# Kernel optimization log

Hardware: AMD Instinct MI355X
Metric: run time of the kernel (lower is better)

Reference implementation:

```python
import jax, jax.numpy as jnp
import numpy as np

INPUT_DIM = 512
SLOT_DIM = 256
MEM_SLOTS = 64

def setup_inputs() -> dict:
    key = jax.random.key(0)
    ks = jax.random.split(key, 6)
    B, S = 16, 4096
    sequence = jax.random.normal(ks[0], (B, S, INPUT_DIM), dtype=jnp.float32)
    # encoder Linear(input_dim -> slot_dim)
    enc_w = jax.random.normal(ks[1], (SLOT_DIM, INPUT_DIM), dtype=jnp.float32) / np.sqrt(INPUT_DIM)
    enc_b = jnp.zeros((SLOT_DIM,), dtype=jnp.float32)
    # memory bank
    mem = jax.random.normal(ks[2], (MEM_SLOTS, SLOT_DIM), dtype=jnp.float32) * 0.1
    # decoder Linear(slot_dim -> input_dim)
    dec_w = jax.random.normal(ks[3], (INPUT_DIM, SLOT_DIM), dtype=jnp.float32) / np.sqrt(SLOT_DIM)
    dec_b = jnp.zeros((INPUT_DIM,), dtype=jnp.float32)
    return {"sequence": sequence, "enc_w": enc_w, "enc_b": enc_b,
            "mem": mem, "dec_w": dec_w, "dec_b": dec_b}

def reference(sequence, enc_w, enc_b, mem, dec_w, dec_b):
    # encode: [B,S,D] @ [D,Dk] -> tanh
    encoded = jnp.tanh(jnp.einsum('bsd,kd->bsk', sequence, enc_w) + enc_b)
    scale = jnp.sqrt(jnp.asarray(encoded.shape[-1], encoded.dtype))
    # attention over memory slots: [B,S,M]
    attention = jax.nn.softmax(jnp.einsum('bsk,mk->bsm', encoded, mem) / scale, axis=-1)
    # weighted read: [B,S,Dk]
    memory = jnp.einsum('bsm,mk->bsk', attention, mem)
    # decode: [B,S,D]
    reconstruction = jnp.einsum('bsk,dk->bsd', memory, dec_w) + dec_b
    return reconstruction, attention, memory
```

## Files before the change

kernel.cpp:

```cpp
#include <hip/hip_runtime.h>

#define IN_DIM  512
#define SL_DIM  256
#define M_SLOTS 64
#define TILE_R  64

typedef __attribute__((ext_vector_type(8))) short  short8;
typedef __attribute__((ext_vector_type(4))) float  f32x4;

__device__ __forceinline__ short f2bf(float f) {
  union { float f; unsigned u; } v; v.f = f;
  unsigned r = (v.u + 0x7FFFu + ((v.u >> 16) & 1u)) >> 16;
  return (short)r;
}

__device__ __forceinline__ float fast_tanh(float x) {
  x = fminf(15.f, fmaxf(-15.f, x));
  float e = __expf(2.f * x);
  return (e - 1.f) / (e + 1.f);
}

__global__ void convert_weights(const float* __restrict__ enc_w,
                                const float* __restrict__ dec_w,
                                const float* __restrict__ mem,
                                short* __restrict__ encb, short* __restrict__ decb,
                                short* __restrict__ memb, short* __restrict__ memTb) {
  int i = blockIdx.x * 256 + threadIdx.x;
  encb[i] = f2bf(enc_w[i]);
  decb[i] = f2bf(dec_w[i]);
  if (i < M_SLOTS * SL_DIM) {
    short v = f2bf(mem[i]);
    memb[i] = v;
    memTb[(i & 255) * M_SLOTS + (i >> 8)] = v;
  }
}

__global__ __launch_bounds__(256, 3) void fused_kernel(
    const float* __restrict__ seq, const float* __restrict__ enc_b,
    const float* __restrict__ dec_b, const short* __restrict__ encw,
    const short* __restrict__ decw, const short* __restrict__ memb,
    const short* __restrict__ memTb, float* __restrict__ out) {
  const int tid  = threadIdx.x;
  const int wave = tid >> 6;
  const int lane = tid & 63;
  const int l16  = lane & 15;
  const int quad = lane >> 4;
  const int r0   = blockIdx.x * TILE_R;

  __shared__ __align__(16) short As[TILE_R][40];
  __shared__ __align__(16) short Ebuf[TILE_R][SL_DIM + 8];
  __shared__ __align__(16) short Pbuf[TILE_R][M_SLOTS + 8];

  float* __restrict__ outR = out;
  float* __restrict__ outA = out + 33554432;
  float* __restrict__ outM = out + 37748736;

  f32x4 acc[4][4];
#pragma unroll
  for (int rb = 0; rb < 4; ++rb)
#pragma unroll
    for (int cb = 0; cb < 4; ++cb) acc[rb][cb] = (f32x4){0.f, 0.f, 0.f, 0.f};

  const int srow = tid >> 2;
  const int skc  = (tid & 3) * 8;
  const float* sp = seq + (size_t)(r0 + srow) * IN_DIM + skc;

  for (int kt = 0; kt < 16; ++kt) {
    const int k0 = kt * 32;
    float4 v0 = *(const float4*)(sp + k0);
    float4 v1 = *(const float4*)(sp + k0 + 4);
    short8 s;
    s[0] = f2bf(v0.x); s[1] = f2bf(v0.y); s[2] = f2bf(v0.z); s[3] = f2bf(v0.w);
    s[4] = f2bf(v1.x); s[5] = f2bf(v1.y); s[6] = f2bf(v1.z); s[7] = f2bf(v1.w);
    __syncthreads();
    *(short8*)&As[srow][skc] = s;
    __syncthreads();
    short8 a[4], b[4];
#pragma unroll
    for (int rb = 0; rb < 4; ++rb)
      a[rb] = *(const short8*)&As[16 * rb + l16][quad * 8];
#pragma unroll
    for (int cb = 0; cb < 4; ++cb) {
      int n = 64 * wave + 16 * cb + l16;
      b[cb] = *(const short8*)(encw + n * IN_DIM + k0 + quad * 8);
    }
#pragma unroll
    for (int rb = 0; rb < 4; ++rb)
#pragma unroll
      for (int cb = 0; cb < 4; ++cb)
        acc[rb][cb] = __builtin_amdgcn_mfma_f32_16x16x32_bf16(a[rb], b[cb], acc[rb][cb], 0, 0, 0);
  }

#pragma unroll
  for (int cb = 0; cb < 4; ++cb) {
    int col = 64 * wave + 16 * cb + l16;
    float bias = enc_b[col];
#pragma unroll
    for (int rb = 0; rb < 4; ++rb)
#pragma unroll
      for (int r = 0; r < 4; ++r) {
        int row = 16 * rb + quad * 4 + r;
        Ebuf[row][col] = f2bf(fast_tanh(acc[rb][cb][r] + bias));
      }
  }
  __syncthreads();

  f32x4 acc2[4];
#pragma unroll
  for (int nb = 0; nb < 4; ++nb) acc2[nb] = (f32x4){0.f, 0.f, 0.f, 0.f};
  const int g2row = 16 * wave + l16;
#pragma unroll
  for (int kt = 0; kt < 8; ++kt) {
    int k0 = kt * 32;
    short8 a = *(const short8*)&Ebuf[g2row][k0 + quad * 8];
#pragma unroll
    for (int nb = 0; nb < 4; ++nb) {
      short8 b = *(const short8*)(memb + (16 * nb + l16) * SL_DIM + k0 + quad * 8);
      acc2[nb] = __builtin_amdgcn_mfma_f32_16x16x32_bf16(a, b, acc2[nb], 0, 0, 0);
    }
  }
#pragma unroll
  for (int r = 0; r < 4; ++r) {
    int lrow = 16 * wave + quad * 4 + r;
    float s0 = acc2[0][r] * 0.0625f, s1 = acc2[1][r] * 0.0625f;
    float s2 = acc2[2][r] * 0.0625f, s3 = acc2[3][r] * 0.0625f;
    float mx = fmaxf(fmaxf(s0, s1), fmaxf(s2, s3));
    for (int off = 1; off < 16; off <<= 1) mx = fmaxf(mx, __shfl_xor(mx, off));
    float e0 = __expf(s0 - mx), e1 = __expf(s1 - mx);
    float e2 = __expf(s2 - mx), e3 = __expf(s3 - mx);
    float sum = e0 + e1 + e2 + e3;
    for (int off = 1; off < 16; off <<= 1) sum += __shfl_xor(sum, off);
    float inv = 1.0f / sum;
    float p0 = e0 * inv, p1 = e1 * inv, p2 = e2 * inv, p3 = e3 * inv;
    size_t grow = (size_t)(r0 + lrow) * M_SLOTS;
    outA[grow + 0  + l16] = p0;  Pbuf[lrow][0  + l16] = f2bf(p0);
    outA[grow + 16 + l16] = p1;  Pbuf[lrow][16 + l16] = f2bf(p1);
    outA[grow + 32 + l16] = p2;  Pbuf[lrow][32 + l16] = f2bf(p2);
    outA[grow + 48 + l16] = p3;  Pbuf[lrow][48 + l16] = f2bf(p3);
  }
  __syncthreads();

  f32x4 acc3[4][4];
#pragma unroll
  for (int rb = 0; rb < 4; ++rb)
#pragma unroll
    for (int cb = 0; cb < 4; ++cb) acc3[rb][cb] = (f32x4){0.f, 0.f, 0.f, 0.f};
#pragma unroll
  for (int kt = 0; kt < 2; ++kt) {
    int k0 = kt * 32;
    short8 a[4], b[4];
#pragma unroll
    for (int rb = 0; rb < 4; ++rb)
      a[rb] = *(const short8*)&Pbuf[16 * rb + l16][k0 + quad * 8];
#pragma unroll
    for (int cb = 0; cb < 4; ++cb) {
      int n = 64 * wave + 16 * cb + l16;
      b[cb] = *(const short8*)(memTb + n * M_SLOTS + k0 + quad * 8);
    }
#pragma unroll
    for (int rb = 0; rb < 4; ++rb)
#pragma unroll
      for (int cb = 0; cb < 4; ++cb)
        acc3[rb][cb] = __builtin_amdgcn_mfma_f32_16x16x32_bf16(a[rb], b[cb], acc3[rb][cb], 0, 0, 0);
  }
#pragma unroll
  for (int cb = 0; cb < 4; ++cb) {
    int col = 64 * wave + 16 * cb + l16;
#pragma unroll
    for (int rb = 0; rb < 4; ++rb)
#pragma unroll
      for (int r = 0; r < 4; ++r) {
        int row = 16 * rb + quad * 4 + r;
        float v = acc3[rb][cb][r];
        outM[(size_t)(r0 + row) * SL_DIM + col] = v;
        Ebuf[row][col] = f2bf(v);
      }
  }
  __syncthreads();

  for (int h = 0; h < 2; ++h) {
    const int c0 = 128 * wave + 64 * h;
    f32x4 acc4[4][4];
#pragma unroll
    for (int rb = 0; rb < 4; ++rb)
#pragma unroll
      for (int cb = 0; cb < 4; ++cb) acc4[rb][cb] = (f32x4){0.f, 0.f, 0.f, 0.f};
#pragma unroll
    for (int kt = 0; kt < 8; ++kt) {
      int k0 = kt * 32;
      short8 a[4], b[4];
#pragma unroll
      for (int rb = 0; rb < 4; ++rb)
        a[rb] = *(const short8*)&Ebuf[16 * rb + l16][k0 + quad * 8];
#pragma unroll
      for (int cb = 0; cb < 4; ++cb) {
        int n = c0 + 16 * cb + l16;
        b[cb] = *(const short8*)(decw + n * SL_DIM + k0 + quad * 8);
      }
#pragma unroll
      for (int rb = 0; rb < 4; ++rb)
#pragma unroll
        for (int cb = 0; cb < 4; ++cb)
          acc4[rb][cb] = __builtin_amdgcn_mfma_f32_16x16x32_bf16(a[rb], b[cb], acc4[rb][cb], 0, 0, 0);
    }
#pragma unroll
    for (int cb = 0; cb < 4; ++cb) {
      int col = c0 + 16 * cb + l16;
      float bias = dec_b[col];
#pragma unroll
      for (int rb = 0; rb < 4; ++rb)
#pragma unroll
        for (int r = 0; r < 4; ++r) {
          int row = 16 * rb + quad * 4 + r;
          outR[(size_t)(r0 + row) * IN_DIM + col] = acc4[rb][cb][r] + bias;
        }
    }
  }
}

extern "C" void kernel_launch(void* const* d_in, const int* in_sizes, int n_in,
                              void* d_out, int out_size, void* d_ws, size_t ws_size,
                              hipStream_t stream) {
  const float* seq   = (const float*)d_in[0];
  const float* enc_w = (const float*)d_in[1];
  const float* enc_b = (const float*)d_in[2];
  const float* mem   = (const float*)d_in[3];
  const float* dec_w = (const float*)d_in[4];
  const float* dec_b = (const float*)d_in[5];
  float* out = (float*)d_out;

  char* ws = (char*)d_ws;
  short* encb  = (short*)(ws);
  short* decb  = (short*)(ws + 262144);
  short* memb  = (short*)(ws + 524288);
  short* memTb = (short*)(ws + 557056);

  convert_weights<<<512, 256, 0, stream>>>(enc_w, dec_w, mem, encb, decb, memb, memTb);
  fused_kernel<<<1024, 256, 0, stream>>>(seq, enc_b, dec_b, encb, decb, memb, memTb, out);
}
```

Measured before the change: 396.8 us.

## Load sequence A-fragments directly from global, dropping LDS staging and barriers

The encoder GEMM no longer stages the fp32 sequence tile through shared memory with two barriers per k-step. Each wave now loads its own A fragments straight from global memory and packs them to bf16 with the paired hardware conversion intrinsic. This removes per-iteration __syncthreads and LDS traffic. The cost is that every wave re-reads the same 64x32 sequence slice, so global/L2 load volume for the sequence rises fourfold and conversion work is duplicated across waves.

```diff
diff --git a/kernel.cpp b/kernel.cpp
--- a/kernel.cpp
+++ b/kernel.cpp
@@ -1,4 +1,5 @@
 #include <hip/hip_runtime.h>
+#include <hip/hip_bf16.h>
 
 #define IN_DIM  512
 #define SL_DIM  256
@@ -12,6 +13,21 @@
   union { float f; unsigned u; } v; v.f = f;
   unsigned r = (v.u + 0x7FFFu + ((v.u >> 16) & 1u)) >> 16;
   return (short)r;
+}
+
+__device__ __forceinline__ unsigned cvt2(float lo, float hi) {
+  union { __hip_bfloat162 h; unsigned u; } c;
+  c.h = __float22bfloat162_rn(make_float2(lo, hi));
+  return c.u;
+}
+
+__device__ __forceinline__ short8 pack8(float4 v0, float4 v1) {
+  union { unsigned u[4]; short8 s; } r;
+  r.u[0] = cvt2(v0.x, v0.y);
+  r.u[1] = cvt2(v0.z, v0.w);
+  r.u[2] = cvt2(v1.x, v1.y);
+  r.u[3] = cvt2(v1.z, v1.w);
+  return r.s;
 }
 
 __device__ __forceinline__ float fast_tanh(float x) {
@@ -47,7 +63,6 @@
   const int quad = lane >> 4;
   const int r0   = blockIdx.x * TILE_R;
 
-  __shared__ __align__(16) short As[TILE_R][40];
   __shared__ __align__(16) short Ebuf[TILE_R][SL_DIM + 8];
   __shared__ __align__(16) short Pbuf[TILE_R][M_SLOTS + 8];
 
@@ -61,29 +76,27 @@
 #pragma unroll
     for (int cb = 0; cb < 4; ++cb) acc[rb][cb] = (f32x4){0.f, 0.f, 0.f, 0.f};
 
-  const int srow = tid >> 2;
-  const int skc  = (tid & 3) * 8;
-  const float* sp = seq + (size_t)(r0 + srow) * IN_DIM + skc;
+  const float* aP[4];
+  const short* bP[4];
+#pragma unroll
+  for (int rb = 0; rb < 4; ++rb)
+    aP[rb] = seq + (size_t)(r0 + 16 * rb + l16) * IN_DIM + quad * 8;
+#pragma unroll
+  for (int cb = 0; cb < 4; ++cb)
+    bP[cb] = encw + (64 * wave + 16 * cb + l16) * IN_DIM + quad * 8;
 
   for (int kt = 0; kt < 16; ++kt) {
     const int k0 = kt * 32;
-    float4 v0 = *(const float4*)(sp + k0);
-    float4 v1 = *(const float4*)(sp + k0 + 4);
-    short8 s;
-    s[0] = f2bf(v0.x); s[1] = f2bf(v0.y); s[2] = f2bf(v0.z); s[3] = f2bf(v0.w);
-    s[4] = f2bf(v1.x); s[5] = f2bf(v1.y); s[6] = f2bf(v1.z); s[7] = f2bf(v1.w);
-    __syncthreads();
-    *(short8*)&As[srow][skc] = s;
-    __syncthreads();
     short8 a[4], b[4];
 #pragma unroll
-    for (int rb = 0; rb < 4; ++rb)
-      a[rb] = *(const short8*)&As[16 * rb + l16][quad * 8];
-#pragma unroll
-    for (int cb = 0; cb < 4; ++cb) {
-      int n = 64 * wave + 16 * cb + l16;
-      b[cb] = *(const short8*)(encw + n * IN_DIM + k0 + quad * 8);
-    }
+    for (int rb = 0; rb < 4; ++rb) {
+      float4 v0 = *(const float4*)(aP[rb] + k0);
+      float4 v1 = *(const float4*)(aP[rb] + k0 + 4);
+      a[rb] = pack8(v0, v1);
+    }
+#pragma unroll
+    for (int cb = 0; cb < 4; ++cb)
+      b[cb] = *(const short8*)(bP[cb] + k0);
 #pragma unroll
     for (int rb = 0; rb < 4; ++rb)
 #pragma unroll
```

Result: slower. 420.9 us (+6.1%).
